# Kernel optimization log

Measured on AMD Instinct MI355X. Metric: run time of the kernel, lower is better.

The kernel has to match this reference:

```python
import jax, jax.numpy as jnp
import numpy as np

SAMPLE_RATE = 16000
FREQ_LOW = 200.0
FREQ_HIGH = 1200.0
# deterministic stand-in for random.uniform(freq_low, freq_high): midpoint
FREQUENCY = 0.5 * (FREQ_LOW + FREQ_HIGH)  # 700 Hz
CUTOFF = FREQUENCY / SAMPLE_RATE          # normalized cutoff, as in cutoff_frequency()
Q = 0.70710678  # standard Butterworth-like quality factor for biquad highpass


def _biquad_highpass_coeffs(cutoff, q):
    # standard audio-EQ-cookbook highpass biquad, cutoff normalized to sample rate
    w0 = 2.0 * np.pi * cutoff
    cw, sw = np.cos(w0), np.sin(w0)
    alpha = sw / (2.0 * q)
    b0 = (1.0 + cw) / 2.0
    b1 = -(1.0 + cw)
    b2 = (1.0 + cw) / 2.0
    a0 = 1.0 + alpha
    a1 = -2.0 * cw
    a2 = 1.0 - alpha
    return (np.float32(b0 / a0), np.float32(b1 / a0), np.float32(b2 / a0),
            np.float32(a1 / a0), np.float32(a2 / a0))


def setup_inputs() -> dict:
    key = jax.random.key(0)
    B, C, T = 128, 2, 65536
    audio = jax.random.normal(key, (B, C, T), dtype=jnp.float32)
    return {"audio": audio}


def reference(audio) -> jnp.ndarray:
    b0, b1, b2, a1, a2 = _biquad_highpass_coeffs(CUTOFF, Q)
    x_t = jnp.moveaxis(audio, -1, 0)  # [T, B, C] for scan over time
    zero = jnp.zeros(x_t.shape[1:], dtype=audio.dtype)

    def step(carry, x):
        x1, x2, y1, y2 = carry
        # IIR biquad difference equation
        y = b0 * x + b1 * x1 + b2 * x2 - a1 * y1 - a2 * y2
        return (x, x1, y, y1), y

    _, y_t = jax.lax.scan(step, (zero, zero, zero, zero), x_t)
    return jnp.moveaxis(y_t, 0, -1)  # [B, C, T]
```

## Files before the change

### kernel.cpp

```cpp
#include <hip/hip_runtime.h>
#include <math.h>


#define T_LEN   65536
#define L_CHUNK 64
#define W_WARM  64
#define TS      32
#define BLK     256
#define NT      ((W_WARM + L_CHUNK) / TS)
#define CHUNK_SHIFT 10
#define ROWS    64
#define WLDS    (ROWS * TS)

__device__ __forceinline__ void lds_fence() {
    asm volatile("s_waitcnt lgkmcnt(0)" ::: "memory");
}

__device__ __forceinline__ void load_tile(const float* __restrict__ x,
                                          int cg0, int tile, float4 pf[8],
                                          int lane)
{
    #pragma unroll
    for (int p = 0; p < 8; ++p) {
        int q   = lane + (p << 6);
        int seg = q >> 3;
        int g   = q & 7;
        int cg  = cg0 + seg;
        int pos = cg * L_CHUNK - W_WARM + tile * TS + (g << 2);
        int cbase = (cg >> CHUNK_SHIFT) * T_LEN;
        float4 v = make_float4(0.f, 0.f, 0.f, 0.f);
        if (pos >= cbase)
            v = *(const float4*)(x + pos);
        pf[p] = v;
    }
}

__global__ __launch_bounds__(BLK, 4)
void hp_biquad_kernel(const float* __restrict__ x, float* __restrict__ y,
                      float b0, float b1, float b2, float a1, float a2)
{
    __shared__ float lds[4 * WLDS];
    const int tid  = threadIdx.x;
    const int lane = tid & 63;
    const int wv   = tid >> 6;
    float* wlds = lds + wv * WLDS;

    const int cg0 = (blockIdx.x * 4 + wv) * ROWS;

    float x1 = 0.f, x2 = 0.f, y1 = 0.f, y2 = 0.f;
    float4 pf[8];

    load_tile(x, cg0, 0, pf, lane);

    for (int tile = 0; tile < NT; ++tile) {
        #pragma unroll
        for (int p = 0; p < 8; ++p) {
            int q    = lane + (p << 6);
            int seg  = q >> 3;
            int g    = q & 7;
            int slot = ((g + seg) & 7) << 2;
            *(float4*)&wlds[seg * TS + slot] = pf[p];
        }
        lds_fence();

        if (tile + 1 < NT)
            load_tile(x, cg0, tile + 1, pf, lane);

        #pragma unroll
        for (int g = 0; g < 8; ++g) {
            int slot = ((g + lane) & 7) << 2;
            float4 v = *(float4*)&wlds[lane * TS + slot];
            float yv;
            yv = b0 * v.x + b1 * x1 + b2 * x2 - a1 * y1 - a2 * y2;
            x2 = x1; x1 = v.x; y2 = y1; y1 = yv; v.x = yv;
            yv = b0 * v.y + b1 * x1 + b2 * x2 - a1 * y1 - a2 * y2;
            x2 = x1; x1 = v.y; y2 = y1; y1 = yv; v.y = yv;
            yv = b0 * v.z + b1 * x1 + b2 * x2 - a1 * y1 - a2 * y2;
            x2 = x1; x1 = v.z; y2 = y1; y1 = yv; v.z = yv;
            yv = b0 * v.w + b1 * x1 + b2 * x2 - a1 * y1 - a2 * y2;
            x2 = x1; x1 = v.w; y2 = y1; y1 = yv; v.w = yv;
            *(float4*)&wlds[lane * TS + slot] = v;
        }
        lds_fence();

        if (tile >= W_WARM / TS) {
            #pragma unroll
            for (int p = 0; p < 8; ++p) {
                int q    = lane + (p << 6);
                int seg  = q >> 3;
                int g    = q & 7;
                int slot = ((g + seg) & 7) << 2;
                float4 v = *(float4*)&wlds[seg * TS + slot];
                int cg   = cg0 + seg;
                int pos  = cg * L_CHUNK - W_WARM + tile * TS + (g << 2);
                *(float4*)(y + pos) = v;
            }
            lds_fence();
        }
    }
}

extern "C" void kernel_launch(void* const* d_in, const int* in_sizes, int n_in,
                              void* d_out, int out_size, void* d_ws, size_t ws_size,
                              hipStream_t stream)
{
    const float* x = (const float*)d_in[0];
    float* y = (float*)d_out;

    const double SR = 16000.0, FLO = 200.0, FHI = 1200.0;
    const double freq   = 0.5 * (FLO + FHI);
    const double cutoff = freq / SR;
    const double q      = 0.70710678;
    const double w0 = 2.0 * M_PI * cutoff;
    const double cw = cos(w0), sw = sin(w0);
    const double alpha = sw / (2.0 * q);
    const double b0 = (1.0 + cw) / 2.0;
    const double b1 = -(1.0 + cw);
    const double b2 = (1.0 + cw) / 2.0;
    const double a0 = 1.0 + alpha;
    const double a1 = -2.0 * cw;
    const double a2 = 1.0 - alpha;
    const float fb0 = (float)(b0 / a0), fb1 = (float)(b1 / a0), fb2 = (float)(b2 / a0);
    const float fa1 = (float)(a1 / a0), fa2 = (float)(a2 / a0);

    const int total  = 128 * 2 * T_LEN;
    const int chunks = total / L_CHUNK;
    const int blocks = chunks / BLK;

    hp_biquad_kernel<<<blocks, BLK, 0, stream>>>(x, y, fb0, fb1, fb2, fa1, fa2);
    (void)in_sizes; (void)n_in; (void)out_size; (void)d_ws; (void)ws_size;
}
```

Before: 118.6 us.

## Use single-wave blocks with double-buffered prefetch and skip LDS writeback in warmup

Blocks shrink from four waves to one, so each block gets its own small LDS tile and a per-block cbase is computed once. Global loads are now prefetched two tiles ahead using a double register buffer, and the tile loop is fully unrolled. Each lane reads its whole LDS row into registers before running the recurrence, and results go back to LDS only for non-warmup tiles. The intent is more memory latency hiding and fewer LDS round trips, at the cost of higher register pressure (two buffers of 8 float4 plus 8 more) and many more, smaller blocks.

```diff
diff --git a/kernel.cpp b/kernel.cpp
--- a/kernel.cpp
+++ b/kernel.cpp
@@ -6,7 +6,7 @@
 #define L_CHUNK 64
 #define W_WARM  64
 #define TS      32
-#define BLK     256
+#define BLK     64
 #define NT      ((W_WARM + L_CHUNK) / TS)
 #define CHUNK_SHIFT 10
 #define ROWS    64
@@ -17,17 +17,15 @@
 }
 
 __device__ __forceinline__ void load_tile(const float* __restrict__ x,
-                                          int cg0, int tile, float4 pf[8],
-                                          int lane)
+                                          int cg0, int cbase, int tile,
+                                          float4* pf, int lane)
 {
     #pragma unroll
     for (int p = 0; p < 8; ++p) {
         int q   = lane + (p << 6);
         int seg = q >> 3;
         int g   = q & 7;
-        int cg  = cg0 + seg;
-        int pos = cg * L_CHUNK - W_WARM + tile * TS + (g << 2);
-        int cbase = (cg >> CHUNK_SHIFT) * T_LEN;
+        int pos = (cg0 + seg) * L_CHUNK - W_WARM + tile * TS + (g << 2);
         float4 v = make_float4(0.f, 0.f, 0.f, 0.f);
         if (pos >= cbase)
             v = *(const float4*)(x + pos);
@@ -39,37 +37,44 @@
 void hp_biquad_kernel(const float* __restrict__ x, float* __restrict__ y,
                       float b0, float b1, float b2, float a1, float a2)
 {
-    __shared__ float lds[4 * WLDS];
-    const int tid  = threadIdx.x;
-    const int lane = tid & 63;
-    const int wv   = tid >> 6;
-    float* wlds = lds + wv * WLDS;
+    __shared__ float wlds[WLDS];
+    const int lane = threadIdx.x;
+    const int cg0  = blockIdx.x * ROWS;
+    const int cbase = (cg0 >> CHUNK_SHIFT) * T_LEN;
 
-    const int cg0 = (blockIdx.x * 4 + wv) * ROWS;
+    float4 pf[2][8];
+    load_tile(x, cg0, cbase, 0, pf[0], lane);
+    load_tile(x, cg0, cbase, 1, pf[1], lane);
 
     float x1 = 0.f, x2 = 0.f, y1 = 0.f, y2 = 0.f;
-    float4 pf[8];
 
-    load_tile(x, cg0, 0, pf, lane);
+    #pragma unroll
+    for (int tile = 0; tile < NT; ++tile) {
+        float4* cur = pf[tile & 1];
 
-    for (int tile = 0; tile < NT; ++tile) {
         #pragma unroll
         for (int p = 0; p < 8; ++p) {
             int q    = lane + (p << 6);
             int seg  = q >> 3;
             int g    = q & 7;
             int slot = ((g + seg) & 7) << 2;
-            *(float4*)&wlds[seg * TS + slot] = pf[p];
+            *(float4*)&wlds[seg * TS + slot] = cur[p];
         }
         lds_fence();
 
-        if (tile + 1 < NT)
-            load_tile(x, cg0, tile + 1, pf, lane);
+        if (tile + 2 < NT)
+            load_tile(x, cg0, cbase, tile + 2, cur, lane);
+
+        float4 r[8];
+        #pragma unroll
+        for (int g = 0; g < 8; ++g) {
+            int slot = ((g + lane) & 7) << 2;
+            r[g] = *(float4*)&wlds[lane * TS + slot];
+        }
 
         #pragma unroll
         for (int g = 0; g < 8; ++g) {
-            int slot = ((g + lane) & 7) << 2;
-            float4 v = *(float4*)&wlds[lane * TS + slot];
+            float4 v = r[g];
             float yv;
             yv = b0 * v.x + b1 * x1 + b2 * x2 - a1 * y1 - a2 * y2;
             x2 = x1; x1 = v.x; y2 = y1; y1 = yv; v.x = yv;
@@ -79,11 +84,16 @@
             x2 = x1; x1 = v.z; y2 = y1; y1 = yv; v.z = yv;
             yv = b0 * v.w + b1 * x1 + b2 * x2 - a1 * y1 - a2 * y2;
             x2 = x1; x1 = v.w; y2 = y1; y1 = yv; v.w = yv;
-            *(float4*)&wlds[lane * TS + slot] = v;
+            r[g] = v;
         }
-        lds_fence();
 
         if (tile >= W_WARM / TS) {
+            #pragma unroll
+            for (int g = 0; g < 8; ++g) {
+                int slot = ((g + lane) & 7) << 2;
+                *(float4*)&wlds[lane * TS + slot] = r[g];
+            }
+            lds_fence();
             #pragma unroll
             for (int p = 0; p < 8; ++p) {
                 int q    = lane + (p << 6);
@@ -91,12 +101,11 @@
                 int g    = q & 7;
                 int slot = ((g + seg) & 7) << 2;
                 float4 v = *(float4*)&wlds[seg * TS + slot];
-                int cg   = cg0 + seg;
-                int pos  = cg * L_CHUNK - W_WARM + tile * TS + (g << 2);
+                int pos  = (cg0 + seg) * L_CHUNK - W_WARM + tile * TS + (g << 2);
                 *(float4*)(y + pos) = v;
             }
-            lds_fence();
         }
+        lds_fence();
     }
 }
 
```

Measured after the change: 134.0 us. +13.0%, slower.
